# Kernel optimization log

Hardware: AMD Instinct MI355X
Metric: run time of the kernel (lower is better)

Reference implementation:

```python
import jax, jax.numpy as jnp
import numpy as np

N_DATA, N_SYN, IN_DIM, OUT_DIM = 128, 8, 784, 128


def setup_inputs() -> dict:
    key = jax.random.key(0)
    k1, k2, k3, k4 = jax.random.split(key, 4)
    # input in the module's assumed input_range (-1, 1)
    x = jax.random.uniform(k1, (N_DATA, IN_DIM), jnp.float32, minval=-1.0, maxval=1.0)
    # thres ~ U(-1, 1) per input_range=(-1, 1)
    thres = jax.random.uniform(k2, (N_SYN, IN_DIM, OUT_DIM), jnp.float32, minval=-1.0, maxval=1.0)
    # slope ~ 10 * U(0, 1)
    slope = 10.0 * jax.random.uniform(k3, (N_SYN, IN_DIM, OUT_DIM), jnp.float32)
    # ampli ~ U(0, 1)
    ampli = jax.random.uniform(k4, (N_SYN, IN_DIM, OUT_DIM), jnp.float32)
    return {"x": x, "thres": thres, "slope": slope, "ampli": ampli}


def reference(x, thres, slope, ampli):
    # z: (n_data, n_synapse, input_dim, output_dim) broadcast affine
    z = slope[None, :, :, :] * x[:, None, :, None] - thres[None, :, :, :]
    # sum over synapse and input dims, weighted by ampli**2
    out = jnp.einsum("nsio,sio->no", jnp.tanh(z), ampli * ampli)
    return out  # (n_data, output_dim)
```

## Files before the change

### kernel.cpp

```cpp
#include <hip/hip_runtime.h>


#define N_DATA  128
#define N_SYN   8
#define IN_DIM  784
#define OUT_DIM 128

#define NTILE   32
#define NACC    16
#define ICHUNK  14
#define NICHUNK 56
#define NTILES  4

__global__ __launch_bounds__(256)
void psl_kernel(const float* __restrict__ x,
                const float* __restrict__ thres,
                const float* __restrict__ slope,
                const float* __restrict__ ampli,
                float* __restrict__ out)
{
    const int t    = threadIdx.x;
    const int o    = t & 127;
    const int nsub = t >> 7;

    int bid = blockIdx.x;
    const int ic    = bid % NICHUNK; bid /= NICHUNK;
    const int s     = bid % N_SYN;   bid /= N_SYN;
    const int ntile = bid;

    const int i0    = ic * ICHUNK;
    const int nbase = ntile * NTILE + nsub * NACC;

    __shared__ float xs[ICHUNK][NTILE];

    for (int idx = t; idx < ICHUNK * NTILE; idx += 256) {
        const int nl = idx & (NTILE - 1);
        const int il = idx >> 5;
        xs[il][nl] = x[(ntile * NTILE + nl) * IN_DIM + i0 + il];
    }
    __syncthreads();

    float acc[NACC];
#pragma unroll
    for (int k = 0; k < NACC; ++k) acc[k] = 0.f;
    float suma2 = 0.f;

    const float C = 2.8853900817779268f;
    const int pbase = (s * IN_DIM + i0) * OUT_DIM + o;

#pragma unroll
    for (int il = 0; il < ICHUNK; ++il) {
        const int pidx = pbase + il * OUT_DIM;
        const float sl = slope[pidx];
        const float th = thres[pidx];
        const float am = ampli[pidx];

        const float a2   = am * am;
        suma2 += a2;
        const float m2a2 = -2.f * a2;
        const float slC  = sl * C;
        const float thC  = th * C;

        const float4* xrow = reinterpret_cast<const float4*>(&xs[il][nsub * NACC]);
#pragma unroll
        for (int q = 0; q < 4; ++q) {
            const float4 xv = xrow[q];
            {
                float z = __builtin_fmaf(slC, xv.x, -thC);
                float r = __builtin_amdgcn_rcpf(__builtin_amdgcn_exp2f(z) + 1.f);
                acc[4*q+0] = __builtin_fmaf(m2a2, r, acc[4*q+0]);
            }
            {
                float z = __builtin_fmaf(slC, xv.y, -thC);
                float r = __builtin_amdgcn_rcpf(__builtin_amdgcn_exp2f(z) + 1.f);
                acc[4*q+1] = __builtin_fmaf(m2a2, r, acc[4*q+1]);
            }
            {
                float z = __builtin_fmaf(slC, xv.z, -thC);
                float r = __builtin_amdgcn_rcpf(__builtin_amdgcn_exp2f(z) + 1.f);
                acc[4*q+2] = __builtin_fmaf(m2a2, r, acc[4*q+2]);
            }
            {
                float z = __builtin_fmaf(slC, xv.w, -thC);
                float r = __builtin_amdgcn_rcpf(__builtin_amdgcn_exp2f(z) + 1.f);
                acc[4*q+3] = __builtin_fmaf(m2a2, r, acc[4*q+3]);
            }
        }
    }

#pragma unroll
    for (int k = 0; k < NACC; ++k) {
        atomicAdd(&out[(nbase + k) * OUT_DIM + o], acc[k] + suma2);
    }
}

extern "C" void kernel_launch(void* const* d_in, const int* in_sizes, int n_in,
                              void* d_out, int out_size, void* d_ws, size_t ws_size,
                              hipStream_t stream) {
    const float* x     = (const float*)d_in[0];
    const float* thres = (const float*)d_in[1];
    const float* slope = (const float*)d_in[2];
    const float* ampli = (const float*)d_in[3];
    float* out = (float*)d_out;

    hipMemsetAsync(out, 0, (size_t)out_size * sizeof(float), stream);

    const int nblocks = NTILES * N_SYN * NICHUNK;
    psl_kernel<<<nblocks, 256, 0, stream>>>(x, thres, slope, ampli, out);
}
```

Before: 101.3 us.

## Replace global atomic accumulation with workspace partials and a separate reduction kernel

```diff
diff --git a/kernel.cpp b/kernel.cpp
--- a/kernel.cpp
+++ b/kernel.cpp
@@ -11,13 +11,15 @@
 #define ICHUNK  14
 #define NICHUNK 56
 #define NTILES  4
+#define NBLK1   (NTILES * N_SYN * NICHUNK)
+#define FANIN   (N_SYN * NICHUNK)
 
 __global__ __launch_bounds__(256)
-void psl_kernel(const float* __restrict__ x,
+void psl_phase1(const float* __restrict__ x,
                 const float* __restrict__ thres,
                 const float* __restrict__ slope,
                 const float* __restrict__ ampli,
-                float* __restrict__ out)
+                float* __restrict__ ws)
 {
     const int t    = threadIdx.x;
     const int o    = t & 127;
@@ -28,11 +30,9 @@
     const int s     = bid % N_SYN;   bid /= N_SYN;
     const int ntile = bid;
 
-    const int i0    = ic * ICHUNK;
-    const int nbase = ntile * NTILE + nsub * NACC;
+    const int i0 = ic * ICHUNK;
 
     __shared__ float xs[ICHUNK][NTILE];
-
     for (int idx = t; idx < ICHUNK * NTILE; idx += 256) {
         const int nl = idx & (NTILE - 1);
         const int il = idx >> 5;
@@ -88,10 +88,38 @@
         }
     }
 
+    float* wsb = ws + (size_t)blockIdx.x * (NTILE * OUT_DIM);
 #pragma unroll
     for (int k = 0; k < NACC; ++k) {
-        atomicAdd(&out[(nbase + k) * OUT_DIM + o], acc[k] + suma2);
+        wsb[(nsub * NACC + k) * OUT_DIM + o] = acc[k] + suma2;
     }
+}
+
+__global__ __launch_bounds__(256)
+void psl_phase2(const float* __restrict__ ws,
+                float* __restrict__ out)
+{
+    const int t = threadIdx.x;
+    const int o = t & 127;
+    const int h = t >> 7;
+    const int n = blockIdx.x;
+    const int ntile = n >> 5;
+    const int nl    = n & 31;
+
+    __shared__ float red[OUT_DIM];
+
+    const float* p = ws + (((size_t)(ntile * FANIN + h * (FANIN / 2)) * NTILE + nl) * OUT_DIM) + o;
+    const size_t stride = (size_t)NTILE * OUT_DIM;
+
+    float sum = 0.f;
+#pragma unroll 8
+    for (int m = 0; m < FANIN / 2; ++m) {
+        sum += p[m * stride];
+    }
+
+    if (h == 1) red[o] = sum;
+    __syncthreads();
+    if (h == 0) out[n * OUT_DIM + o] = sum + red[o];
 }
 
 extern "C" void kernel_launch(void* const* d_in, const int* in_sizes, int n_in,
@@ -102,9 +130,8 @@
     const float* slope = (const float*)d_in[2];
     const float* ampli = (const float*)d_in[3];
     float* out = (float*)d_out;
+    float* ws  = (float*)d_ws;
 
-    hipMemsetAsync(out, 0, (size_t)out_size * sizeof(float), stream);
-
-    const int nblocks = NTILES * N_SYN * NICHUNK;
-    psl_kernel<<<nblocks, 256, 0, stream>>>(x, thres, slope, ampli, out);
+    psl_phase1<<<NBLK1, 256, 0, stream>>>(x, thres, slope, ampli, ws);
+    psl_phase2<<<N_DATA, 256, 0, stream>>>(ws, out);
 }
```

Measured after the change: 102.6 us. About the same (+1.2%).
